# Optimization experiments

Measured on AMD Instinct MI355X. Metric: run time of the kernel, lower is better.

## Reference

```python
import jax, jax.numpy as jnp
import numpy as np

N_PTS = 65536   # input points
M = 4096        # sampled clusters (n_nodes)
K = 16          # knn neighbors
C_IN = 128
C_OUT = 256
BN_EPS = 1e-5


def setup_inputs() -> dict:
    key = jax.random.key(0)
    k1, k2, k3 = jax.random.split(key, 3)
    x = jax.random.normal(k1, (N_PTS, C_IN), jnp.float32)
    pos = jax.random.normal(k2, (N_PTS, 3), jnp.float32)
    batch = jnp.zeros((N_PTS,), jnp.int32)  # single point cloud
    W = jax.random.normal(k3, (C_IN, C_OUT), jnp.float32) / np.sqrt(C_IN)
    b = jnp.zeros((C_OUT,), jnp.float32)
    gamma = jnp.ones((C_OUT,), jnp.float32)
    beta = jnp.zeros((C_OUT,), jnp.float32)
    return {"x": x, "pos": pos, "batch": batch, "W": W, "b": b,
            "gamma": gamma, "beta": beta}


def _fps(pos, m):
    """Farthest point sampling starting from index 0. Returns m indices."""
    n = pos.shape[0]

    def step(carry, _):
        min_d, last = carry
        d = jnp.sum((pos - pos[last]) ** 2, axis=-1)  # [N]
        min_d = jnp.minimum(min_d, d)
        nxt = jnp.argmax(min_d).astype(jnp.int32)
        return (min_d, nxt), nxt

    init = (jnp.full((n,), jnp.inf, pos.dtype), jnp.int32(0))
    _, rest = jax.lax.scan(step, init, None, length=m - 1)
    return jnp.concatenate([jnp.zeros((1,), jnp.int32), rest])


def _knn(pos, sub_pos, k):
    """For each of M query points, indices of k nearest points in pos. [M, k]"""
    # squared euclidean distances, [M, N]
    d2 = (jnp.sum(sub_pos ** 2, -1, keepdims=True)
          - 2.0 * sub_pos @ pos.T
          + jnp.sum(pos ** 2, -1)[None, :])
    _, idx = jax.lax.top_k(-d2, k)
    return idx


def _mlp(x, W, b, gamma, beta):
    # Linear -> BatchNorm1d (training-mode batch stats, biased var) -> ReLU
    h = x @ W + b                      # [N, C_OUT]
    mu = jnp.mean(h, axis=0)
    var = jnp.mean((h - mu) ** 2, axis=0)
    h = gamma * (h - mu) * jax.lax.rsqrt(var + BN_EPS) + beta
    return jax.nn.relu(h)


def reference(x, pos, batch, W, b, gamma, beta):
    id_clusters = _fps(pos, M)                 # [M]
    sub_pos = pos[id_clusters]                 # [M, 3]
    sub_batch = batch[id_clusters]             # [M]
    nbr = _knn(pos, sub_pos, K)                # [M, K]
    h = _mlp(x, W, b, gamma, beta)             # [N, C_OUT]
    # gather + max-pool over each cluster's k neighbors (== scatter_max,
    # since knn emits exactly K neighbors per cluster, grouped by cluster)
    out = jnp.max(h[nbr], axis=1)              # [M, C_OUT]
    return out, sub_pos, sub_batch
```

## Files before the change

kernel.cpp:

```cpp
#include <hip/hip_runtime.h>
#include <hip/hip_bf16.h>

#define N_PTS 65536
#define MCLUS 4096
#define KNN   16
#define C_IN  128
#define C_OUT 256

typedef unsigned long long u64;
typedef unsigned u32;

#define WS_ID     0
#define WS_SLOTS  16384
#define WS_BBOX   49152
#define WS_CNT    49216
#define WS_OFS    180288
#define WS_NBR    49216
#define WS_POS4   311360
#define WS_PSUM   311360
#define WS_PSUMSQ 835648
#define WS_SCALE  1359936
#define WS_SHIFT  1360960

__device__ __forceinline__ u32 fkey(float v) {
    u32 u = __float_as_uint(v);
    return (u >> 31) ? ~u : (u | 0x80000000u);
}
__device__ __forceinline__ float funkey(u32 k) {
    u32 u = (k >> 31) ? (k & 0x7FFFFFFFu) : ~k;
    return __uint_as_float(u);
}

__global__ void init_kernel(int* __restrict__ id, u64* __restrict__ slots,
                            u32* __restrict__ bbox, int* __restrict__ cellcnt) {
    int t = threadIdx.x;
    for (int i = t; i < 4096; i += 1024) slots[i] = 0ull;
    for (int i = t; i < 32768; i += 1024) cellcnt[i] = 0;
    if (t < 3)   bbox[t] = 0xFFFFFFFFu;
    if (t >= 3 && t < 6) bbox[t] = 0u;
    if (t == 0) id[0] = 0;
}

__global__ __launch_bounds__(256) void bbox_kernel(const float* __restrict__ pos,
                                                   u32* __restrict__ bbox) {
    int t = blockIdx.x * 256 + threadIdx.x;
    u32 mn0 = 0xFFFFFFFFu, mn1 = 0xFFFFFFFFu, mn2 = 0xFFFFFFFFu;
    u32 mx0 = 0u, mx1 = 0u, mx2 = 0u;
    for (int i = t; i < N_PTS; i += 16384) {
        u32 k0 = fkey(pos[i*3+0]), k1 = fkey(pos[i*3+1]), k2 = fkey(pos[i*3+2]);
        mn0 = min(mn0, k0); mn1 = min(mn1, k1); mn2 = min(mn2, k2);
        mx0 = max(mx0, k0); mx1 = max(mx1, k1); mx2 = max(mx2, k2);
    }
    #pragma unroll
    for (int off = 32; off > 0; off >>= 1) {
        mn0 = min(mn0, (u32)__shfl_xor(mn0, off)); mx0 = max(mx0, (u32)__shfl_xor(mx0, off));
        mn1 = min(mn1, (u32)__shfl_xor(mn1, off)); mx1 = max(mx1, (u32)__shfl_xor(mx1, off));
        mn2 = min(mn2, (u32)__shfl_xor(mn2, off)); mx2 = max(mx2, (u32)__shfl_xor(mx2, off));
    }
    if ((threadIdx.x & 63) == 0) {
        atomicMin(&bbox[0], mn0); atomicMin(&bbox[1], mn1); atomicMin(&bbox[2], mn2);
        atomicMax(&bbox[3], mx0); atomicMax(&bbox[4], mx1); atomicMax(&bbox[5], mx2);
    }
}

__device__ __forceinline__ int cell_of(float x, float y, float z, const u32* bb) {
    float x0 = funkey(bb[0]), y0 = funkey(bb[1]), z0 = funkey(bb[2]);
    float x1 = funkey(bb[3]), y1 = funkey(bb[4]), z1 = funkey(bb[5]);
    float sx = 32.0f / fmaxf(x1 - x0, 1e-20f);
    float sy = 32.0f / fmaxf(y1 - y0, 1e-20f);
    float sz = 32.0f / fmaxf(z1 - z0, 1e-20f);
    int gx = min(max((int)((x - x0) * sx), 0), 31);
    int gy = min(max((int)((y - y0) * sy), 0), 31);
    int gz = min(max((int)((z - z0) * sz), 0), 31);
    int m = 0;
    #pragma unroll
    for (int k = 0; k < 5; ++k)
        m |= (((gx >> k) & 1) << (3*k + 2)) | (((gy >> k) & 1) << (3*k + 1)) | (((gz >> k) & 1) << (3*k));
    return m;
}

__global__ __launch_bounds__(256) void count_kernel(const float* __restrict__ pos,
                                                    const u32* __restrict__ bbox,
                                                    int* __restrict__ cellcnt) {
    int i = blockIdx.x * 256 + threadIdx.x;
    atomicAdd(&cellcnt[cell_of(pos[i*3+0], pos[i*3+1], pos[i*3+2], bbox)], 1);
}

__global__ __launch_bounds__(1024) void scan_kernel(const int* __restrict__ cellcnt,
                                                    int* __restrict__ cellofs) {
    __shared__ int ts[1024];
    int t = threadIdx.x;
    int v[32]; int s = 0;
    #pragma unroll
    for (int i = 0; i < 32; ++i) { v[i] = cellcnt[t*32 + i]; s += v[i]; }
    ts[t] = s; __syncthreads();
    for (int off = 1; off < 1024; off <<= 1) {
        int u = (t >= off) ? ts[t - off] : 0;
        __syncthreads();
        ts[t] += u;
        __syncthreads();
    }
    int pre = (t == 0) ? 0 : ts[t - 1];
    #pragma unroll
    for (int i = 0; i < 32; ++i) { cellofs[t*32 + i] = pre; pre += v[i]; }
}

__global__ __launch_bounds__(256) void scatter_kernel(const float* __restrict__ pos,
                                                      const u32* __restrict__ bbox,
                                                      int* __restrict__ cellofs,
                                                      float4* __restrict__ pos4) {
    int i = blockIdx.x * 256 + threadIdx.x;
    float x = pos[i*3+0], y = pos[i*3+1], z = pos[i*3+2];
    int o = atomicAdd(&cellofs[cell_of(x, y, z, bbox)], 1);
    pos4[o] = make_float4(x, y, z, __int_as_float(i));
}

__device__ __forceinline__ float dist3(float ax, float ay, float az,
                                       float bx, float by, float bz) {
    float dx = __fsub_rn(ax, bx), dy = __fsub_rn(ay, by), dz = __fsub_rn(az, bz);
    return __fadd_rn(__fadd_rn(__fmul_rn(dx, dx), __fmul_rn(dy, dy)), __fmul_rn(dz, dz));
}

__device__ __forceinline__ u32 wave_max_u32(u32 v) {
    #pragma unroll
    for (int off = 32; off > 0; off >>= 1) {
        u32 o = __shfl_xor(v, off);
        v = o > v ? o : v;
    }
    return v;
}
__device__ __forceinline__ u32 wave_min_u32(u32 v) {
    #pragma unroll
    for (int off = 32; off > 0; off >>= 1) {
        u32 o = __shfl_xor(v, off);
        v = o < v ? o : v;
    }
    return v;
}

__device__ __forceinline__ int wave_argmax48(u64 k48) {
    u32 hi = (u32)(k48 >> 16);
    u32 him = wave_max_u32(hi);
    u64 ball = __ballot(hi == him);
    if (__popcll(ball) > 1) {
        u32 a = (hi == him) ? (u32)(k48 & 0xFFFFull) : 0u;
        u32 am = wave_max_u32(a);
        ball = __ballot((hi == him) && (a == am));
    }
    return __ffsll((long long)ball) - 1;
}

__global__ __launch_bounds__(64) void fps_kernel(const float* __restrict__ pos,
                                                 const float4* __restrict__ pos4,
                                                 int* __restrict__ id,
                                                 u64* __restrict__ slots) {
    const int lane = threadIdx.x;
    const int blk  = blockIdx.x;
    __shared__ float bku[1024];

    float px[16], py[16], pz[16], md[16];
    u32 inv[16];
    const float c0x = pos[0], c0y = pos[1], c0z = pos[2];
    #pragma unroll
    for (int e = 0; e < 16; ++e) {
        int sp = blk * 1024 + (lane >> 3) * 128 + e * 8 + (lane & 7);
        float4 v = pos4[sp];
        px[e] = v.x; py[e] = v.y; pz[e] = v.z;
        inv[e] = 0xFFFFu - (u32)__float_as_int(v.w);
        md[e] = dist3(px[e], py[e], pz[e], c0x, c0y, c0z);
    }

    int r = 0;
    u32 fb_mine = 0xFu;

    auto slow_round = [&](int rr, int s) {
        u64 bk = 0; float bx = 0.f, by = 0.f, bz = 0.f;
        #pragma unroll
        for (int e = 0; e < 16; ++e) {
            u64 k = ((u64)__float_as_uint(md[e]) << 16) | inv[e];
            bool bt = k > bk;
            bk = bt ? k : bk; bx = bt ? px[e] : bx; by = bt ? py[e] : by; bz = bt ? pz[e] : bz;
        }
        int src = wave_argmax48(bk);
        float wx = __shfl(bx, src), wy = __shfl(by, src), wz = __shfl(bz, src);
        u64 kb = __shfl(bk, src);

        const u64 tg = (u64)((rr + 1) & 0xFFFF);
        u64* base = &slots[(u32)(rr & 1) * 2048];
        {
            u64 w0 = (kb << 16) | tg;
            u64 w1 = ((u64)__float_as_uint(wx) << 32) | tg;
            u64 w2 = ((u64)__float_as_uint(wy) << 32) | tg;
            u64 w3 = ((u64)__float_as_uint(wz) << 32) | tg;
            u64 wv = (lane == 0) ? w0 : (lane == 1) ? w1 : (lane == 2) ? w2 : w3;
            if (lane < 4)
                __hip_atomic_store(&base[(u32)blk * 32 + (u32)lane], wv,
                                   __ATOMIC_RELAXED, __HIP_MEMORY_SCOPE_AGENT);
        }
        u64* bp = &base[(u32)lane * 32];
        u64 v0, v1, v2, v3;
        for (;;) {
            v0 = __hip_atomic_load(&bp[0], __ATOMIC_RELAXED, __HIP_MEMORY_SCOPE_AGENT);
            v1 = __hip_atomic_load(&bp[1], __ATOMIC_RELAXED, __HIP_MEMORY_SCOPE_AGENT);
            v2 = __hip_atomic_load(&bp[2], __ATOMIC_RELAXED, __HIP_MEMORY_SCOPE_AGENT);
            v3 = __hip_atomic_load(&bp[3], __ATOMIC_RELAXED, __HIP_MEMORY_SCOPE_AGENT);
            u64 bad = ((v0 ^ tg) | (v1 ^ tg) | (v2 ^ tg) | (v3 ^ tg)) & 0xFFFFull;
            if (bad == 0ull) break;
        }
        u64 k2 = v0 >> 16;
        int s2 = wave_argmax48(k2);
        u64 kw = __shfl(k2, s2);
        float cx = __shfl(__uint_as_float((u32)(v1 >> 32)), s2);
        float cy = __shfl(__uint_as_float((u32)(v2 >> 32)), s2);
        float cz = __shfl(__uint_as_float((u32)(v3 >> 32)), s2);
        if (blk == 0 && lane == 0) id[s] = (int)(0xFFFFu - (u32)(kw & 0xFFFFull));
        #pragma unroll
        for (int e = 0; e < 16; ++e)
            md[e] = fminf(md[e], dist3(px[e], py[e], pz[e], cx, cy, cz));
    };

    u64 wk48[8]; float wxa[8], wya[8], wza[8];

    for (int B = 0; B <= 511; ++B) {
        u64 bk = 0; float bx = 0.f, by = 0.f, bz = 0.f;
        #pragma unroll
        for (int e = 0; e < 16; ++e) {
            u64 k = ((u64)__float_as_uint(md[e]) << 16) | inv[e];
            bool bt = k > bk;
            bk = bt ? k : bk; bx = bt ? px[e] : bx; by = bt ? py[e] : by; bz = bt ? pz[e] : bz;
        }
        u64 ks = bk;
        #pragma unroll
        for (int off = 1; off <= 4; off <<= 1) {
            u64 o = __shfl_xor(ks, off);
            if (o > ks) ks = o;
        }
        {
            u64 ball = __ballot(bk == ks);
            int segbase = (lane >> 3) << 3;
            int ssrc = __ffsll((long long)(ball & (0xFFull << segbase))) - 1;
            bx = __shfl(bx, ssrc); by = __shfl(by, ssrc); bz = __shfl(bz, ssrc);
        }

        const u64 tg = (u64)((r + 1) & 0xFFFF);
        u64* base = &slots[(u32)(r & 1) * 2048];
        {
            int c = lane / 3; if (c > 7) c = 7;
            int p = lane - c * 3;
            int srcl = 8 * c;
            u64 kk  = __shfl(ks, srcl);
            float gx = __shfl(bx, srcl), gy = __shfl(by, srcl), gz = __shfl(bz, srcl);
            u32 hi, mid;
            if (p == 0)      { hi = __float_as_uint(gx); mid = (u32)(kk & 0xFFFFull); }
            else if (p == 1) { hi = __float_as_uint(gy); mid = (u32)(kk >> 32) & 0xFFFFu; }
            else             { hi = __float_as_uint(gz); mid = (u32)(kk >> 16) & 0xFFFFu; }
            u64 wd = ((u64)hi << 32) | ((u64)mid << 16) | tg;
            if (lane == 24) wd = ((u64)(fb_mine & 0xFu) << 16) | tg;
            if (lane < 25)
                __hip_atomic_store(&base[(u32)blk * 32 + (u32)lane], wd,
                                   __ATOMIC_RELAXED, __HIP_MEMORY_SCOPE_AGENT);
        }

        u64 w[25]; u32 valid = 0;
        {
            u64* bp = &base[(u32)lane * 32];
            do {
                #pragma unroll
                for (int i = 0; i < 25; ++i)
                    if (!(valid & (1u << i)))
                        w[i] = __hip_atomic_load(&bp[i], __ATOMIC_RELAXED, __HIP_MEMORY_SCOPE_AGENT);
                #pragma unroll
                for (int i = 0; i < 25; ++i)
                    if ((u32)(w[i] & 0xFFFFull) == (u32)tg) valid |= (1u << i);
            } while (valid != 0x1FFFFFFu);
        }
        ++r;

        u32 jstar = wave_min_u32((u32)(w[24] >> 16) & 0xFu);
        if (jstar < 8u) {
            #pragma unroll
            for (int e = 0; e < 16; ++e) md[e] = bku[e * 64 + lane];
            #pragma unroll
            for (int j = 0; j < 8; ++j) {
                if ((u32)j < jstar) {
                    #pragma unroll
                    for (int e = 0; e < 16; ++e)
                        md[e] = fminf(md[e], dist3(px[e], py[e], pz[e], wxa[j], wya[j], wza[j]));
                }
            }
            int sbase = 8 * (B - 1) + 1;
            for (int sub = (int)jstar; sub < 8; ++sub) { slow_round(r, sbase + sub); ++r; }
            fb_mine = 0xFu;
            --B; continue;
        }
        if (B == 511) break;

        float cpx[8], cpy[8], cpz[8], cmdf[8]; u32 cinv[8];
        #pragma unroll
        for (int c = 0; c < 8; ++c) {
            u64 a = w[3 * c], b = w[3 * c + 1], d = w[3 * c + 2];
            cpx[c] = __uint_as_float((u32)(a >> 32));
            cpy[c] = __uint_as_float((u32)(b >> 32));
            cpz[c] = __uint_as_float((u32)(d >> 32));
            cinv[c] = (u32)(a >> 16) & 0xFFFFu;
            u32 mdb = (((u32)(b >> 16) & 0xFFFFu) << 16) | ((u32)(d >> 16) & 0xFFFFu);
            cmdf[c] = __uint_as_float(mdb);
        }

        float pwx = 0.f, pwy = 0.f, pwz = 0.f;
        #pragma unroll
        for (int j = 0; j < 8; ++j) {
            if (j) {
                #pragma unroll
                for (int c = 0; c < 8; ++c)
                    cmdf[c] = fminf(cmdf[c], dist3(cpx[c], cpy[c], cpz[c], pwx, pwy, pwz));
            }
            u64 bk2 = 0; float b2x = 0.f, b2y = 0.f, b2z = 0.f;
            #pragma unroll
            for (int c = 0; c < 8; ++c) {
                u64 k = ((u64)__float_as_uint(cmdf[c]) << 16) | cinv[c];
                bool bt = k > bk2;
                bk2 = bt ? k : bk2; b2x = bt ? cpx[c] : b2x; b2y = bt ? cpy[c] : b2y; b2z = bt ? cpz[c] : b2z;
            }
            int src = wave_argmax48(bk2);
            u64 kw = __shfl(bk2, src);
            float wx = __shfl(b2x, src), wy = __shfl(b2y, src), wz = __shfl(b2z, src);
            wk48[j] = kw; wxa[j] = wx; wya[j] = wy; wza[j] = wz;
            pwx = wx; pwy = wy; pwz = wz;
            if (blk == 0 && lane == 0) id[8 * B + 1 + j] = (int)(0xFFFFu - (u32)(kw & 0xFFFFull));
        }

        #pragma unroll
        for (int e = 0; e < 16; ++e) bku[e * 64 + lane] = md[e];
        u32 vmask = 0;
        #pragma unroll
        for (int j = 0; j < 8; ++j) {
            #pragma unroll
            for (int e = 0; e < 16; ++e) {
                u64 vk = ((u64)__float_as_uint(md[e]) << 16) | inv[e];
                if (vk > wk48[j]) vmask |= (1u << j);
            }
            #pragma unroll
            for (int e = 0; e < 16; ++e)
                md[e] = fminf(md[e], dist3(px[e], py[e], pz[e], wxa[j], wya[j], wza[j]));
        }
        #pragma unroll
        for (int off = 32; off > 0; off >>= 1) vmask |= (u32)__shfl_xor(vmask, off);
        fb_mine = vmask ? (u32)(__ffs(vmask) - 1) : 0xFu;
    }

    for (int s = 4089; s < 4096; ++s) { slow_round(r, s); ++r; }
}

__global__ void subout_kernel(const float* __restrict__ pos, const int* __restrict__ batch,
                              const int* __restrict__ id, float* __restrict__ sub_pos,
                              int* __restrict__ sub_batch) {
    int m = blockIdx.x * blockDim.x + threadIdx.x;
    if (m >= MCLUS) return;
    int idx = id[m];
    sub_pos[m*3+0] = pos[idx*3+0];
    sub_pos[m*3+1] = pos[idx*3+1];
    sub_pos[m*3+2] = pos[idx*3+2];
    sub_batch[m] = batch[idx];
}

__global__ __launch_bounds__(64) void knn_kernel(const float* __restrict__ pos,
                                                 const int* __restrict__ id,
                                                 int* __restrict__ nbr) {
    const int q = blockIdx.x;
    const int lane = threadIdx.x;
    const int qi = id[q];
    const float qx = pos[qi*3+0], qy = pos[qi*3+1], qz = pos[qi*3+2];
    const float nq = __fadd_rn(__fadd_rn(__fmul_rn(qx,qx), __fmul_rn(qy,qy)), __fmul_rn(qz,qz));

    float dl[KNN]; int il[KNN];
    #pragma unroll
    for (int t = 0; t < KNN; ++t) { dl[t] = __builtin_inff(); il[t] = 0x7FFFFFFF; }

    for (int j = lane; j < N_PTS; j += 64) {
        float px = pos[j*3+0], py = pos[j*3+1], pz = pos[j*3+2];
        float npj = __fadd_rn(__fadd_rn(__fmul_rn(px,px), __fmul_rn(py,py)), __fmul_rn(pz,pz));
        float dot = __fadd_rn(__fadd_rn(__fmul_rn(qx,px), __fmul_rn(qy,py)), __fmul_rn(qz,pz));
        float d2  = __fadd_rn(__fsub_rn(nq, __fmul_rn(2.0f, dot)), npj);
        if (d2 < dl[KNN-1] || (d2 == dl[KNN-1] && j < il[KNN-1])) {
            dl[KNN-1] = d2; il[KNN-1] = j;
            #pragma unroll
            for (int t = KNN-1; t > 0; --t) {
                float a = dl[t-1], bq = dl[t];
                int   ai = il[t-1], bi = il[t];
                bool sw = (bq < a) || (bq == a && bi < ai);
                dl[t-1] = sw ? bq : a;  dl[t] = sw ? a : bq;
                il[t-1] = sw ? bi : ai; il[t] = sw ? ai : bi;
            }
        }
    }

    __shared__ float sd[64][KNN];
    __shared__ int   si[64][KNN];
    #pragma unroll
    for (int t = 0; t < KNN; ++t) { sd[lane][t] = dl[t]; si[lane][t] = il[t]; }
    __syncthreads();

    int ptr = 0;
    for (int rr = 0; rr < KNN; ++rr) {
        unsigned long long key = ~0ull;
        if (ptr < KNN) {
            unsigned u = __float_as_uint(sd[lane][ptr]);
            unsigned mu = (u >> 31) ? ~u : (u | 0x80000000u);
            key = ((unsigned long long)mu << 32) | (unsigned)si[lane][ptr];
        }
        unsigned long long m = key;
        #pragma unroll
        for (int off = 32; off > 0; off >>= 1) {
            unsigned long long o = __shfl_xor(m, off);
            if (o < m) m = o;
        }
        if (key == m) ptr++;
        if (lane == 0) nbr[q*KNN + rr] = (int)(m & 0xFFFFFFFFull);
    }
}

__global__ __launch_bounds__(256) void stats_kernel(const float* __restrict__ x,
                                                    const float* __restrict__ W,
                                                    const float* __restrict__ b,
                                                    float* __restrict__ psum,
                                                    float* __restrict__ psumsq) {
    __shared__ float xl[64*128];
    const int tid = threadIdx.x;
    const int cg = (tid & 63) * 4;
    const int rq = tid >> 6;
    float s0=0,s1=0,s2v=0,s3=0, q0=0,q1=0,q2=0,q3=0;
    const float4 bv = *(const float4*)&b[cg];

    for (int t = 0; t < 2; ++t) {
        const size_t row0 = (size_t)blockIdx.x*128 + (size_t)t*64;
        __syncthreads();
        for (int i = tid*4; i < 64*128; i += 1024)
            *(float4*)&xl[i] = *(const float4*)&x[row0*128 + i];
        __syncthreads();

        float acc[16][4];
        #pragma unroll
        for (int rr = 0; rr < 16; ++rr) { acc[rr][0]=bv.x; acc[rr][1]=bv.y; acc[rr][2]=bv.z; acc[rr][3]=bv.w; }

        for (int k4 = 0; k4 < 32; ++k4) {
            float4 w0 = *(const float4*)&W[(k4*4+0)*256 + cg];
            float4 w1 = *(const float4*)&W[(k4*4+1)*256 + cg];
            float4 w2 = *(const float4*)&W[(k4*4+2)*256 + cg];
            float4 w3 = *(const float4*)&W[(k4*4+3)*256 + cg];
            #pragma unroll
            for (int rr = 0; rr < 16; ++rr) {
                float4 xv = *(float4*)&xl[(rq*16+rr)*128 + k4*4];
                acc[rr][0] = fmaf(xv.w,w3.x, fmaf(xv.z,w2.x, fmaf(xv.y,w1.x, fmaf(xv.x,w0.x, acc[rr][0]))));
                acc[rr][1] = fmaf(xv.w,w3.y, fmaf(xv.z,w2.y, fmaf(xv.y,w1.y, fmaf(xv.x,w0.y, acc[rr][1]))));
                acc[rr][2] = fmaf(xv.w,w3.z, fmaf(xv.z,w2.z, fmaf(xv.y,w1.z, fmaf(xv.x,w0.z, acc[rr][2]))));
                acc[rr][3] = fmaf(xv.w,w3.w, fmaf(xv.z,w2.w, fmaf(xv.y,w1.w, fmaf(xv.x,w0.w, acc[rr][3]))));
            }
        }
        #pragma unroll
        for (int rr = 0; rr < 16; ++rr) {
            s0 += acc[rr][0]; q0 = fmaf(acc[rr][0],acc[rr][0],q0);
            s1 += acc[rr][1]; q1 = fmaf(acc[rr][1],acc[rr][1],q1);
            s2v+= acc[rr][2]; q2 = fmaf(acc[rr][2],acc[rr][2],q2);
            s3 += acc[rr][3]; q3 = fmaf(acc[rr][3],acc[rr][3],q3);
        }
    }
    __syncthreads();
    float* red = xl;
    red[rq*256 + cg+0] = s0; red[rq*256 + cg+1] = s1; red[rq*256 + cg+2] = s2v; red[rq*256 + cg+3] = s3;
    red[1024 + rq*256 + cg+0] = q0; red[1024 + rq*256 + cg+1] = q1;
    red[1024 + rq*256 + cg+2] = q2; red[1024 + rq*256 + cg+3] = q3;
    __syncthreads();
    if (rq == 0) {
        #pragma unroll
        for (int c = 0; c < 4; ++c) {
            int ch = cg + c;
            float ss = red[ch] + red[256+ch] + red[512+ch] + red[768+ch];
            float qq = red[1024+ch] + red[1280+ch] + red[1536+ch] + red[1792+ch];
            psum  [blockIdx.x*256 + ch] = ss;
            psumsq[blockIdx.x*256 + ch] = qq;
        }
    }
}

__global__ void finalize_kernel(const float* __restrict__ psum, const float* __restrict__ psumsq,
                                const float* __restrict__ gamma, const float* __restrict__ beta,
                                float* __restrict__ scale, float* __restrict__ shift) {
    int c = threadIdx.x;
    float s = 0.f, s2 = 0.f;
    for (int bl = 0; bl < 512; ++bl) { s += psum[bl*256+c]; s2 += psumsq[bl*256+c]; }
    float mu  = s  / 65536.0f;
    float var = s2 / 65536.0f - mu*mu;
    float inv = rsqrtf(var + 1e-5f);
    float sc = gamma[c] * inv;
    scale[c] = sc;
    shift[c] = beta[c] - mu * sc;
}

__global__ __launch_bounds__(256) void out_kernel(const float* __restrict__ x,
                                                  const float* __restrict__ W,
                                                  const float* __restrict__ b,
                                                  const int* __restrict__ nbr,
                                                  const float* __restrict__ scale,
                                                  const float* __restrict__ shift,
                                                  float* __restrict__ out) {
    __shared__ float xl[16*128];
    __shared__ int nb[16];
    const int tid = threadIdx.x;
    const int m = blockIdx.x;
    if (tid < 16) nb[tid] = nbr[m*16 + tid];
    __syncthreads();
    for (int i = tid; i < 16*128; i += 256) {
        int rr = i >> 7, k = i & 127;
        xl[i] = x[(size_t)nb[rr]*128 + k];
    }
    __syncthreads();

    float acc[16];
    const float bias = b[tid];
    #pragma unroll
    for (int rr = 0; rr < 16; ++rr) acc[rr] = bias;

    for (int k4 = 0; k4 < 32; ++k4) {
        float w0 = W[(k4*4+0)*256 + tid];
        float w1 = W[(k4*4+1)*256 + tid];
        float w2 = W[(k4*4+2)*256 + tid];
        float w3 = W[(k4*4+3)*256 + tid];
        #pragma unroll
        for (int rr = 0; rr < 16; ++rr) {
            float4 xv = *(float4*)&xl[rr*128 + k4*4];
            acc[rr] = fmaf(xv.w,w3, fmaf(xv.z,w2, fmaf(xv.y,w1, fmaf(xv.x,w0, acc[rr]))));
        }
    }
    const float sc = scale[tid], sh = shift[tid];
    float v = acc[0];
    #pragma unroll
    for (int rr = 1; rr < 16; ++rr) v = (sc >= 0.f) ? fmaxf(v, acc[rr]) : fminf(v, acc[rr]);
    out[(size_t)m*256 + tid] = fmaxf(fmaf(sc, v, sh), 0.f);
}

extern "C" void kernel_launch(void* const* d_in, const int* in_sizes, int n_in,
                              void* d_out, int out_size, void* d_ws, size_t ws_size,
                              hipStream_t stream) {
    const float* x     = (const float*)d_in[0];
    const float* pos   = (const float*)d_in[1];
    const int*   batch = (const int*)  d_in[2];
    const float* W     = (const float*)d_in[3];
    const float* b     = (const float*)d_in[4];
    const float* gamma = (const float*)d_in[5];
    const float* beta  = (const float*)d_in[6];

    float* out      = (float*)d_out;
    float* sub_pos  = out + (size_t)MCLUS*C_OUT;
    int*   sub_batch= (int*)(out + (size_t)MCLUS*C_OUT + (size_t)MCLUS*3);

    char* ws = (char*)d_ws;
    int*    id      = (int*)   (ws + WS_ID);
    u64*    slots   = (u64*)   (ws + WS_SLOTS);
    u32*    bbox    = (u32*)   (ws + WS_BBOX);
    int*    cellcnt = (int*)   (ws + WS_CNT);
    int*    cellofs = (int*)   (ws + WS_OFS);
    int*    nbr     = (int*)   (ws + WS_NBR);
    float4* pos4    = (float4*)(ws + WS_POS4);
    float*  psum    = (float*) (ws + WS_PSUM);
    float*  psumsq  = (float*) (ws + WS_PSUMSQ);
    float*  scalep  = (float*) (ws + WS_SCALE);
    float*  shiftp  = (float*) (ws + WS_SHIFT);

    init_kernel<<<1, 1024, 0, stream>>>(id, slots, bbox, cellcnt);
    bbox_kernel<<<64, 256, 0, stream>>>(pos, bbox);
    count_kernel<<<256, 256, 0, stream>>>(pos, bbox, cellcnt);
    scan_kernel<<<1, 1024, 0, stream>>>(cellcnt, cellofs);
    scatter_kernel<<<256, 256, 0, stream>>>(pos, bbox, cellofs, pos4);
    fps_kernel<<<64, 64, 0, stream>>>(pos, pos4, id, slots);
    subout_kernel<<<16, 256, 0, stream>>>(pos, batch, id, sub_pos, sub_batch);
    knn_kernel<<<MCLUS, 64, 0, stream>>>(pos, id, nbr);
    stats_kernel<<<512, 256, 0, stream>>>(x, W, b, psum, psumsq);
    finalize_kernel<<<1, 256, 0, stream>>>(psum, psumsq, gamma, beta, scalep, shiftp);
    out_kernel<<<MCLUS, 256, 0, stream>>>(x, W, b, nbr, scalep, shiftp, out);
}
```

Before: 7.829 ms.

## Rewrite FPS as single-block bounding-box-pruned segment update

Replaces the 64-block FPS, which used cross-block atomic slot exchange and speculative 8-step batching, with a single 1024-thread block. Points are split into 512 spatially sorted segments, each with a bounding box and a cached champion. Each step only updates segments whose bounding box lies closer to the new centre than their current max distance. This removes grid-wide spin synchronisation and skips distance updates for unaffected segments. In exchange, all work runs on one CU, min-distances move to global memory, and there are two block barriers per step.

```diff
diff --git a/kernel.cpp b/kernel.cpp
--- a/kernel.cpp
+++ b/kernel.cpp
@@ -9,12 +9,13 @@
 
 typedef unsigned long long u64;
 typedef unsigned u32;
+typedef unsigned short u16;
 
 #define WS_ID     0
-#define WS_SLOTS  16384
-#define WS_BBOX   49152
+#define WS_BBOX   16384
 #define WS_CNT    49216
 #define WS_OFS    180288
+#define WS_MDG    49216
 #define WS_NBR    49216
 #define WS_POS4   311360
 #define WS_PSUM   311360
@@ -31,10 +32,9 @@
     return __uint_as_float(u);
 }
 
-__global__ void init_kernel(int* __restrict__ id, u64* __restrict__ slots,
-                            u32* __restrict__ bbox, int* __restrict__ cellcnt) {
+__global__ void init_kernel(int* __restrict__ id, u32* __restrict__ bbox,
+                            int* __restrict__ cellcnt) {
     int t = threadIdx.x;
-    for (int i = t; i < 4096; i += 1024) slots[i] = 0ull;
     for (int i = t; i < 32768; i += 1024) cellcnt[i] = 0;
     if (t < 3)   bbox[t] = 0xFFFFFFFFu;
     if (t >= 3 && t < 6) bbox[t] = 0u;
@@ -121,235 +121,115 @@
     return __fadd_rn(__fadd_rn(__fmul_rn(dx, dx), __fmul_rn(dy, dy)), __fmul_rn(dz, dz));
 }
 
-__device__ __forceinline__ u32 wave_max_u32(u32 v) {
-    #pragma unroll
-    for (int off = 32; off > 0; off >>= 1) {
-        u32 o = __shfl_xor(v, off);
-        v = o > v ? o : v;
-    }
-    return v;
-}
-__device__ __forceinline__ u32 wave_min_u32(u32 v) {
-    #pragma unroll
-    for (int off = 32; off > 0; off >>= 1) {
-        u32 o = __shfl_xor(v, off);
-        v = o < v ? o : v;
-    }
-    return v;
-}
-
-__device__ __forceinline__ int wave_argmax48(u64 k48) {
-    u32 hi = (u32)(k48 >> 16);
-    u32 him = wave_max_u32(hi);
-    u64 ball = __ballot(hi == him);
-    if (__popcll(ball) > 1) {
-        u32 a = (hi == him) ? (u32)(k48 & 0xFFFFull) : 0u;
-        u32 am = wave_max_u32(a);
-        ball = __ballot((hi == him) && (a == am));
-    }
-    return __ffsll((long long)ball) - 1;
-}
-
-__global__ __launch_bounds__(64) void fps_kernel(const float* __restrict__ pos,
-                                                 const float4* __restrict__ pos4,
-                                                 int* __restrict__ id,
-                                                 u64* __restrict__ slots) {
-    const int lane = threadIdx.x;
-    const int blk  = blockIdx.x;
-    __shared__ float bku[1024];
-
-    float px[16], py[16], pz[16], md[16];
-    u32 inv[16];
+__global__ __launch_bounds__(1024) void fps_kernel(const float* __restrict__ pos,
+                                                   const float4* __restrict__ pos4,
+                                                   float* __restrict__ mdg,
+                                                   int* __restrict__ id) {
+    const int tid = threadIdx.x;
+    const int wave = tid >> 6, lane = tid & 63;
+    __shared__ float bax[512], bay[512], baz[512], bbx[512], bby[512], bbz[512];
+    __shared__ u64 champ[512];
+    __shared__ float chx[512], chy[512], chz[512];
+    __shared__ u16 wl[2][512];
+    __shared__ int wlc[2];
+
     const float c0x = pos[0], c0y = pos[1], c0z = pos[2];
-    #pragma unroll
-    for (int e = 0; e < 16; ++e) {
-        int sp = blk * 1024 + (lane >> 3) * 128 + e * 8 + (lane & 7);
-        float4 v = pos4[sp];
-        px[e] = v.x; py[e] = v.y; pz[e] = v.z;
-        inv[e] = 0xFFFFu - (u32)__float_as_int(v.w);
-        md[e] = dist3(px[e], py[e], pz[e], c0x, c0y, c0z);
-    }
-
-    int r = 0;
-    u32 fb_mine = 0xFu;
-
-    auto slow_round = [&](int rr, int s) {
-        u64 bk = 0; float bx = 0.f, by = 0.f, bz = 0.f;
-        #pragma unroll
-        for (int e = 0; e < 16; ++e) {
-            u64 k = ((u64)__float_as_uint(md[e]) << 16) | inv[e];
-            bool bt = k > bk;
-            bk = bt ? k : bk; bx = bt ? px[e] : bx; by = bt ? py[e] : by; bz = bt ? pz[e] : bz;
-        }
-        int src = wave_argmax48(bk);
-        float wx = __shfl(bx, src), wy = __shfl(by, src), wz = __shfl(bz, src);
-        u64 kb = __shfl(bk, src);
-
-        const u64 tg = (u64)((rr + 1) & 0xFFFF);
-        u64* base = &slots[(u32)(rr & 1) * 2048];
-        {
-            u64 w0 = (kb << 16) | tg;
-            u64 w1 = ((u64)__float_as_uint(wx) << 32) | tg;
-            u64 w2 = ((u64)__float_as_uint(wy) << 32) | tg;
-            u64 w3 = ((u64)__float_as_uint(wz) << 32) | tg;
-            u64 wv = (lane == 0) ? w0 : (lane == 1) ? w1 : (lane == 2) ? w2 : w3;
-            if (lane < 4)
-                __hip_atomic_store(&base[(u32)blk * 32 + (u32)lane], wv,
-                                   __ATOMIC_RELAXED, __HIP_MEMORY_SCOPE_AGENT);
-        }
-        u64* bp = &base[(u32)lane * 32];
-        u64 v0, v1, v2, v3;
-        for (;;) {
-            v0 = __hip_atomic_load(&bp[0], __ATOMIC_RELAXED, __HIP_MEMORY_SCOPE_AGENT);
-            v1 = __hip_atomic_load(&bp[1], __ATOMIC_RELAXED, __HIP_MEMORY_SCOPE_AGENT);
-            v2 = __hip_atomic_load(&bp[2], __ATOMIC_RELAXED, __HIP_MEMORY_SCOPE_AGENT);
-            v3 = __hip_atomic_load(&bp[3], __ATOMIC_RELAXED, __HIP_MEMORY_SCOPE_AGENT);
-            u64 bad = ((v0 ^ tg) | (v1 ^ tg) | (v2 ^ tg) | (v3 ^ tg)) & 0xFFFFull;
-            if (bad == 0ull) break;
-        }
-        u64 k2 = v0 >> 16;
-        int s2 = wave_argmax48(k2);
-        u64 kw = __shfl(k2, s2);
-        float cx = __shfl(__uint_as_float((u32)(v1 >> 32)), s2);
-        float cy = __shfl(__uint_as_float((u32)(v2 >> 32)), s2);
-        float cz = __shfl(__uint_as_float((u32)(v3 >> 32)), s2);
-        if (blk == 0 && lane == 0) id[s] = (int)(0xFFFFu - (u32)(kw & 0xFFFFull));
-        #pragma unroll
-        for (int e = 0; e < 16; ++e)
-            md[e] = fminf(md[e], dist3(px[e], py[e], pz[e], cx, cy, cz));
-    };
-
-    u64 wk48[8]; float wxa[8], wya[8], wza[8];
-
-    for (int B = 0; B <= 511; ++B) {
-        u64 bk = 0; float bx = 0.f, by = 0.f, bz = 0.f;
-        #pragma unroll
-        for (int e = 0; e < 16; ++e) {
-            u64 k = ((u64)__float_as_uint(md[e]) << 16) | inv[e];
-            bool bt = k > bk;
-            bk = bt ? k : bk; bx = bt ? px[e] : bx; by = bt ? py[e] : by; bz = bt ? pz[e] : bz;
-        }
-        u64 ks = bk;
-        #pragma unroll
-        for (int off = 1; off <= 4; off <<= 1) {
-            u64 o = __shfl_xor(ks, off);
-            if (o > ks) ks = o;
-        }
-        {
-            u64 ball = __ballot(bk == ks);
-            int segbase = (lane >> 3) << 3;
-            int ssrc = __ffsll((long long)(ball & (0xFFull << segbase))) - 1;
-            bx = __shfl(bx, ssrc); by = __shfl(by, ssrc); bz = __shfl(bz, ssrc);
-        }
-
-        const u64 tg = (u64)((r + 1) & 0xFFFF);
-        u64* base = &slots[(u32)(r & 1) * 2048];
-        {
-            int c = lane / 3; if (c > 7) c = 7;
-            int p = lane - c * 3;
-            int srcl = 8 * c;
-            u64 kk  = __shfl(ks, srcl);
-            float gx = __shfl(bx, srcl), gy = __shfl(by, srcl), gz = __shfl(bz, srcl);
-            u32 hi, mid;
-            if (p == 0)      { hi = __float_as_uint(gx); mid = (u32)(kk & 0xFFFFull); }
-            else if (p == 1) { hi = __float_as_uint(gy); mid = (u32)(kk >> 32) & 0xFFFFu; }
-            else             { hi = __float_as_uint(gz); mid = (u32)(kk >> 16) & 0xFFFFu; }
-            u64 wd = ((u64)hi << 32) | ((u64)mid << 16) | tg;
-            if (lane == 24) wd = ((u64)(fb_mine & 0xFu) << 16) | tg;
-            if (lane < 25)
-                __hip_atomic_store(&base[(u32)blk * 32 + (u32)lane], wd,
-                                   __ATOMIC_RELAXED, __HIP_MEMORY_SCOPE_AGENT);
-        }
-
-        u64 w[25]; u32 valid = 0;
-        {
-            u64* bp = &base[(u32)lane * 32];
-            do {
-                #pragma unroll
-                for (int i = 0; i < 25; ++i)
-                    if (!(valid & (1u << i)))
-                        w[i] = __hip_atomic_load(&bp[i], __ATOMIC_RELAXED, __HIP_MEMORY_SCOPE_AGENT);
-                #pragma unroll
-                for (int i = 0; i < 25; ++i)
-                    if ((u32)(w[i] & 0xFFFFull) == (u32)tg) valid |= (1u << i);
-            } while (valid != 0x1FFFFFFu);
-        }
-        ++r;
-
-        u32 jstar = wave_min_u32((u32)(w[24] >> 16) & 0xFu);
-        if (jstar < 8u) {
+
+    for (int seg = wave; seg < 512; seg += 16) {
+        int p0 = seg*128 + lane, p1 = p0 + 64;
+        float4 a = pos4[p0], b = pos4[p1];
+        float m0 = dist3(a.x, a.y, a.z, c0x, c0y, c0z);
+        float m1 = dist3(b.x, b.y, b.z, c0x, c0y, c0z);
+        mdg[p0] = m0; mdg[p1] = m1;
+        float xn = fminf(a.x,b.x), xM = fmaxf(a.x,b.x);
+        float yn = fminf(a.y,b.y), yM = fmaxf(a.y,b.y);
+        float zn = fminf(a.z,b.z), zM = fmaxf(a.z,b.z);
+        u64 k0 = ((u64)__float_as_uint(m0) << 16) | (0xFFFFu - (u32)__float_as_int(a.w));
+        u64 k1 = ((u64)__float_as_uint(m1) << 16) | (0xFFFFu - (u32)__float_as_int(b.w));
+        bool t = k1 > k0;
+        u64 kk = t ? k1 : k0;
+        float qx = t ? b.x : a.x, qy = t ? b.y : a.y, qz = t ? b.z : a.z;
+        #pragma unroll
+        for (int off = 32; off > 0; off >>= 1) {
+            xn = fminf(xn, (float)__shfl_xor(xn, off)); xM = fmaxf(xM, (float)__shfl_xor(xM, off));
+            yn = fminf(yn, (float)__shfl_xor(yn, off)); yM = fmaxf(yM, (float)__shfl_xor(yM, off));
+            zn = fminf(zn, (float)__shfl_xor(zn, off)); zM = fmaxf(zM, (float)__shfl_xor(zM, off));
+            u64 ok = __shfl_xor(kk, off);
+            float ox = __shfl_xor(qx, off), oy = __shfl_xor(qy, off), oz = __shfl_xor(qz, off);
+            if (ok > kk) { kk = ok; qx = ox; qy = oy; qz = oz; }
+        }
+        if (lane == 0) {
+            bax[seg] = xn; bbx[seg] = xM;
+            bay[seg] = yn; bby[seg] = yM;
+            baz[seg] = zn; bbz[seg] = zM;
+            champ[seg] = kk; chx[seg] = qx; chy[seg] = qy; chz[seg] = qz;
+        }
+    }
+    if (tid == 0) { id[0] = 0; wlc[0] = 0; wlc[1] = 0; }
+    __syncthreads();
+
+    for (int s = 1; s < 4096; ++s) {
+        const int buf = s & 1;
+        u64 kmax = 0; int kseg = 0;
+        #pragma unroll
+        for (int i = 0; i < 8; ++i) {
+            u64 k = champ[lane + 64*i];
+            if (k > kmax) { kmax = k; kseg = lane + 64*i; }
+        }
+        #pragma unroll
+        for (int off = 32; off > 0; off >>= 1) {
+            u64 ok = __shfl_xor(kmax, off);
+            int os = __shfl_xor(kseg, off);
+            if (ok > kmax) { kmax = ok; kseg = os; }
+        }
+        const float cx = chx[kseg], cy = chy[kseg], cz = chz[kseg];
+        if (tid == 0) id[s] = (int)(0xFFFFu - (u32)(kmax & 0xFFFFull));
+        if (s == 4095) break;
+
+        if (tid < 512) {
+            float ddx = fmaxf(fmaxf(bax[tid] - cx, cx - bbx[tid]), 0.f);
+            float ddy = fmaxf(fmaxf(bay[tid] - cy, cy - bby[tid]), 0.f);
+            float ddz = fmaxf(fmaxf(baz[tid] - cz, cz - bbz[tid]), 0.f);
+            float dbb = ddx*ddx + ddy*ddy + ddz*ddz;
+            float cm  = __uint_as_float((u32)(champ[tid] >> 16));
+            bool aff = dbb < cm * 1.00002f;
+            u64 ball = __ballot(aff);
+            int nb = __popcll(ball);
+            int pre = __popcll(ball & ((1ull << lane) - 1ull));
+            int base = 0;
+            if (lane == 0 && nb) base = atomicAdd(&wlc[buf], nb);
+            base = __shfl(base, 0);
+            if (aff) wl[buf][base + pre] = (u16)tid;
+        }
+        if (tid == 0) wlc[buf ^ 1] = 0;
+        __syncthreads();
+
+        const int n = wlc[buf];
+        for (int i = wave; i < n; i += 16) {
+            int seg = wl[buf][i];
+            int p0 = seg*128 + lane, p1 = p0 + 64;
+            float4 a = pos4[p0]; float m0 = mdg[p0];
+            float4 b = pos4[p1]; float m1 = mdg[p1];
+            m0 = fminf(m0, dist3(a.x, a.y, a.z, cx, cy, cz));
+            m1 = fminf(m1, dist3(b.x, b.y, b.z, cx, cy, cz));
+            mdg[p0] = m0; mdg[p1] = m1;
+            u64 k0 = ((u64)__float_as_uint(m0) << 16) | (0xFFFFu - (u32)__float_as_int(a.w));
+            u64 k1 = ((u64)__float_as_uint(m1) << 16) | (0xFFFFu - (u32)__float_as_int(b.w));
+            bool t = k1 > k0;
+            u64 kk = t ? k1 : k0;
+            float qx = t ? b.x : a.x, qy = t ? b.y : a.y, qz = t ? b.z : a.z;
             #pragma unroll
-            for (int e = 0; e < 16; ++e) md[e] = bku[e * 64 + lane];
-            #pragma unroll
-            for (int j = 0; j < 8; ++j) {
-                if ((u32)j < jstar) {
-                    #pragma unroll
-                    for (int e = 0; e < 16; ++e)
-                        md[e] = fminf(md[e], dist3(px[e], py[e], pz[e], wxa[j], wya[j], wza[j]));
-                }
+            for (int off = 32; off > 0; off >>= 1) {
+                u64 ok = __shfl_xor(kk, off);
+                float ox = __shfl_xor(qx, off), oy = __shfl_xor(qy, off), oz = __shfl_xor(qz, off);
+                if (ok > kk) { kk = ok; qx = ox; qy = oy; qz = oz; }
             }
-            int sbase = 8 * (B - 1) + 1;
-            for (int sub = (int)jstar; sub < 8; ++sub) { slow_round(r, sbase + sub); ++r; }
-            fb_mine = 0xFu;
-            --B; continue;
-        }
-        if (B == 511) break;
-
-        float cpx[8], cpy[8], cpz[8], cmdf[8]; u32 cinv[8];
-        #pragma unroll
-        for (int c = 0; c < 8; ++c) {
-            u64 a = w[3 * c], b = w[3 * c + 1], d = w[3 * c + 2];
-            cpx[c] = __uint_as_float((u32)(a >> 32));
-            cpy[c] = __uint_as_float((u32)(b >> 32));
-            cpz[c] = __uint_as_float((u32)(d >> 32));
-            cinv[c] = (u32)(a >> 16) & 0xFFFFu;
-            u32 mdb = (((u32)(b >> 16) & 0xFFFFu) << 16) | ((u32)(d >> 16) & 0xFFFFu);
-            cmdf[c] = __uint_as_float(mdb);
-        }
-
-        float pwx = 0.f, pwy = 0.f, pwz = 0.f;
-        #pragma unroll
-        for (int j = 0; j < 8; ++j) {
-            if (j) {
-                #pragma unroll
-                for (int c = 0; c < 8; ++c)
-                    cmdf[c] = fminf(cmdf[c], dist3(cpx[c], cpy[c], cpz[c], pwx, pwy, pwz));
+            if (lane == 0) {
+                champ[seg] = kk; chx[seg] = qx; chy[seg] = qy; chz[seg] = qz;
             }
-            u64 bk2 = 0; float b2x = 0.f, b2y = 0.f, b2z = 0.f;
-            #pragma unroll
-            for (int c = 0; c < 8; ++c) {
-                u64 k = ((u64)__float_as_uint(cmdf[c]) << 16) | cinv[c];
-                bool bt = k > bk2;
-                bk2 = bt ? k : bk2; b2x = bt ? cpx[c] : b2x; b2y = bt ? cpy[c] : b2y; b2z = bt ? cpz[c] : b2z;
-            }
-            int src = wave_argmax48(bk2);
-            u64 kw = __shfl(bk2, src);
-            float wx = __shfl(b2x, src), wy = __shfl(b2y, src), wz = __shfl(b2z, src);
-            wk48[j] = kw; wxa[j] = wx; wya[j] = wy; wza[j] = wz;
-            pwx = wx; pwy = wy; pwz = wz;
-            if (blk == 0 && lane == 0) id[8 * B + 1 + j] = (int)(0xFFFFu - (u32)(kw & 0xFFFFull));
-        }
-
-        #pragma unroll
-        for (int e = 0; e < 16; ++e) bku[e * 64 + lane] = md[e];
-        u32 vmask = 0;
-        #pragma unroll
-        for (int j = 0; j < 8; ++j) {
-            #pragma unroll
-            for (int e = 0; e < 16; ++e) {
-                u64 vk = ((u64)__float_as_uint(md[e]) << 16) | inv[e];
-                if (vk > wk48[j]) vmask |= (1u << j);
-            }
-            #pragma unroll
-            for (int e = 0; e < 16; ++e)
-                md[e] = fminf(md[e], dist3(px[e], py[e], pz[e], wxa[j], wya[j], wza[j]));
-        }
-        #pragma unroll
-        for (int off = 32; off > 0; off >>= 1) vmask |= (u32)__shfl_xor(vmask, off);
-        fb_mine = vmask ? (u32)(__ffs(vmask) - 1) : 0xFu;
-    }
-
-    for (int s = 4089; s < 4096; ++s) { slow_round(r, s); ++r; }
+        }
+        __syncthreads();
+    }
 }
 
 __global__ void subout_kernel(const float* __restrict__ pos, const int* __restrict__ batch,
@@ -556,10 +436,10 @@
 
     char* ws = (char*)d_ws;
     int*    id      = (int*)   (ws + WS_ID);
-    u64*    slots   = (u64*)   (ws + WS_SLOTS);
     u32*    bbox    = (u32*)   (ws + WS_BBOX);
     int*    cellcnt = (int*)   (ws + WS_CNT);
     int*    cellofs = (int*)   (ws + WS_OFS);
+    float*  mdg     = (float*) (ws + WS_MDG);
     int*    nbr     = (int*)   (ws + WS_NBR);
     float4* pos4    = (float4*)(ws + WS_POS4);
     float*  psum    = (float*) (ws + WS_PSUM);
@@ -567,12 +447,12 @@
     float*  scalep  = (float*) (ws + WS_SCALE);
     float*  shiftp  = (float*) (ws + WS_SHIFT);
 
-    init_kernel<<<1, 1024, 0, stream>>>(id, slots, bbox, cellcnt);
+    init_kernel<<<1, 1024, 0, stream>>>(id, bbox, cellcnt);
     bbox_kernel<<<64, 256, 0, stream>>>(pos, bbox);
     count_kernel<<<256, 256, 0, stream>>>(pos, bbox, cellcnt);
     scan_kernel<<<1, 1024, 0, stream>>>(cellcnt, cellofs);
     scatter_kernel<<<256, 256, 0, stream>>>(pos, bbox, cellofs, pos4);
-    fps_kernel<<<64, 64, 0, stream>>>(pos, pos4, id, slots);
+    fps_kernel<<<1, 1024, 0, stream>>>(pos, pos4, mdg, id);
     subout_kernel<<<16, 256, 0, stream>>>(pos, batch, id, sub_pos, sub_batch);
     knn_kernel<<<MCLUS, 64, 0, stream>>>(pos, id, nbr);
     stats_kernel<<<512, 256, 0, stream>>>(x, W, b, psum, psumsq);
```

Result: slower. 16.71 ms (+113.4%).

## Replace slow-round fallback with variable-length speculative batches in FPS

Applied to the files above, without the earlier changes.

The persistent FPS kernel now commits only the verified prefix of each speculative batch of 8 picks. It then restarts speculation from that point, instead of falling back to single-pick rounds that each need a full cross-block exchange. The fixed-length block loop and the tail of slow rounds are replaced by a running count of confirmed samples and a variable batch size. This is meant to cut the number of global synchronization rounds after mis-speculation and at the tail. In exchange the control flow is more complex, and a conflict now always costs an extra exchange round before progress resumes.

```diff
diff --git a/kernel.cpp b/kernel.cpp
--- a/kernel.cpp
+++ b/kernel.cpp
@@ -172,56 +172,11 @@
 
     int r = 0;
     u32 fb_mine = 0xFu;
-
-    auto slow_round = [&](int rr, int s) {
-        u64 bk = 0; float bx = 0.f, by = 0.f, bz = 0.f;
-        #pragma unroll
-        for (int e = 0; e < 16; ++e) {
-            u64 k = ((u64)__float_as_uint(md[e]) << 16) | inv[e];
-            bool bt = k > bk;
-            bk = bt ? k : bk; bx = bt ? px[e] : bx; by = bt ? py[e] : by; bz = bt ? pz[e] : bz;
-        }
-        int src = wave_argmax48(bk);
-        float wx = __shfl(bx, src), wy = __shfl(by, src), wz = __shfl(bz, src);
-        u64 kb = __shfl(bk, src);
-
-        const u64 tg = (u64)((rr + 1) & 0xFFFF);
-        u64* base = &slots[(u32)(rr & 1) * 2048];
-        {
-            u64 w0 = (kb << 16) | tg;
-            u64 w1 = ((u64)__float_as_uint(wx) << 32) | tg;
-            u64 w2 = ((u64)__float_as_uint(wy) << 32) | tg;
-            u64 w3 = ((u64)__float_as_uint(wz) << 32) | tg;
-            u64 wv = (lane == 0) ? w0 : (lane == 1) ? w1 : (lane == 2) ? w2 : w3;
-            if (lane < 4)
-                __hip_atomic_store(&base[(u32)blk * 32 + (u32)lane], wv,
-                                   __ATOMIC_RELAXED, __HIP_MEMORY_SCOPE_AGENT);
-        }
-        u64* bp = &base[(u32)lane * 32];
-        u64 v0, v1, v2, v3;
-        for (;;) {
-            v0 = __hip_atomic_load(&bp[0], __ATOMIC_RELAXED, __HIP_MEMORY_SCOPE_AGENT);
-            v1 = __hip_atomic_load(&bp[1], __ATOMIC_RELAXED, __HIP_MEMORY_SCOPE_AGENT);
-            v2 = __hip_atomic_load(&bp[2], __ATOMIC_RELAXED, __HIP_MEMORY_SCOPE_AGENT);
-            v3 = __hip_atomic_load(&bp[3], __ATOMIC_RELAXED, __HIP_MEMORY_SCOPE_AGENT);
-            u64 bad = ((v0 ^ tg) | (v1 ^ tg) | (v2 ^ tg) | (v3 ^ tg)) & 0xFFFFull;
-            if (bad == 0ull) break;
-        }
-        u64 k2 = v0 >> 16;
-        int s2 = wave_argmax48(k2);
-        u64 kw = __shfl(k2, s2);
-        float cx = __shfl(__uint_as_float((u32)(v1 >> 32)), s2);
-        float cy = __shfl(__uint_as_float((u32)(v2 >> 32)), s2);
-        float cz = __shfl(__uint_as_float((u32)(v3 >> 32)), s2);
-        if (blk == 0 && lane == 0) id[s] = (int)(0xFFFFu - (u32)(kw & 0xFFFFull));
-        #pragma unroll
-        for (int e = 0; e < 16; ++e)
-            md[e] = fminf(md[e], dist3(px[e], py[e], pz[e], cx, cy, cz));
-    };
-
+    int s_conf = 0;
+    int nsub = 0;
     u64 wk48[8]; float wxa[8], wya[8], wza[8];
 
-    for (int B = 0; B <= 511; ++B) {
+    for (;;) {
         u64 bk = 0; float bx = 0.f, by = 0.f, bz = 0.f;
         #pragma unroll
         for (int e = 0; e < 16; ++e) {
@@ -277,23 +232,24 @@
         ++r;
 
         u32 jstar = wave_min_u32((u32)(w[24] >> 16) & 0xFu);
-        if (jstar < 8u) {
+        int adv = (jstar < (u32)nsub) ? (int)jstar : nsub;
+        if (adv < nsub) {
             #pragma unroll
             for (int e = 0; e < 16; ++e) md[e] = bku[e * 64 + lane];
             #pragma unroll
             for (int j = 0; j < 8; ++j) {
-                if ((u32)j < jstar) {
+                if (j < adv) {
                     #pragma unroll
                     for (int e = 0; e < 16; ++e)
                         md[e] = fminf(md[e], dist3(px[e], py[e], pz[e], wxa[j], wya[j], wza[j]));
                 }
             }
-            int sbase = 8 * (B - 1) + 1;
-            for (int sub = (int)jstar; sub < 8; ++sub) { slow_round(r, sbase + sub); ++r; }
-            fb_mine = 0xFu;
-            --B; continue;
-        }
-        if (B == 511) break;
+            s_conf += adv; nsub = 0; fb_mine = 0xFu;
+            continue;
+        }
+        s_conf += nsub; nsub = 0; fb_mine = 0xFu;
+        if (s_conf >= 4095) break;
+        nsub = (4095 - s_conf) < 8 ? (4095 - s_conf) : 8;
 
         float cpx[8], cpy[8], cpz[8], cmdf[8]; u32 cinv[8];
         #pragma unroll
@@ -307,49 +263,52 @@
             cmdf[c] = __uint_as_float(mdb);
         }
 
+        #pragma unroll
+        for (int e = 0; e < 16; ++e) bku[e * 64 + lane] = md[e];
+
         float pwx = 0.f, pwy = 0.f, pwz = 0.f;
         #pragma unroll
         for (int j = 0; j < 8; ++j) {
-            if (j) {
+            if (j < nsub) {
+                if (j) {
+                    #pragma unroll
+                    for (int c = 0; c < 8; ++c)
+                        cmdf[c] = fminf(cmdf[c], dist3(cpx[c], cpy[c], cpz[c], pwx, pwy, pwz));
+                }
+                u64 bk2 = 0; float b2x = 0.f, b2y = 0.f, b2z = 0.f;
                 #pragma unroll
-                for (int c = 0; c < 8; ++c)
-                    cmdf[c] = fminf(cmdf[c], dist3(cpx[c], cpy[c], cpz[c], pwx, pwy, pwz));
+                for (int c = 0; c < 8; ++c) {
+                    u64 k = ((u64)__float_as_uint(cmdf[c]) << 16) | cinv[c];
+                    bool bt = k > bk2;
+                    bk2 = bt ? k : bk2; b2x = bt ? cpx[c] : b2x; b2y = bt ? cpy[c] : b2y; b2z = bt ? cpz[c] : b2z;
+                }
+                int src = wave_argmax48(bk2);
+                u64 kw = __shfl(bk2, src);
+                float wx = __shfl(b2x, src), wy = __shfl(b2y, src), wz = __shfl(b2z, src);
+                wk48[j] = kw; wxa[j] = wx; wya[j] = wy; wza[j] = wz;
+                pwx = wx; pwy = wy; pwz = wz;
+                if (blk == 0 && lane == 0) id[s_conf + 1 + j] = (int)(0xFFFFu - (u32)(kw & 0xFFFFull));
             }
-            u64 bk2 = 0; float b2x = 0.f, b2y = 0.f, b2z = 0.f;
-            #pragma unroll
-            for (int c = 0; c < 8; ++c) {
-                u64 k = ((u64)__float_as_uint(cmdf[c]) << 16) | cinv[c];
-                bool bt = k > bk2;
-                bk2 = bt ? k : bk2; b2x = bt ? cpx[c] : b2x; b2y = bt ? cpy[c] : b2y; b2z = bt ? cpz[c] : b2z;
+        }
+
+        u32 vmask = 0;
+        #pragma unroll
+        for (int j = 0; j < 8; ++j) {
+            if (j < nsub) {
+                #pragma unroll
+                for (int e = 0; e < 16; ++e) {
+                    u64 vk = ((u64)__float_as_uint(md[e]) << 16) | inv[e];
+                    if (vk > wk48[j]) vmask |= (1u << j);
+                }
+                #pragma unroll
+                for (int e = 0; e < 16; ++e)
+                    md[e] = fminf(md[e], dist3(px[e], py[e], pz[e], wxa[j], wya[j], wza[j]));
             }
-            int src = wave_argmax48(bk2);
-            u64 kw = __shfl(bk2, src);
-            float wx = __shfl(b2x, src), wy = __shfl(b2y, src), wz = __shfl(b2z, src);
-            wk48[j] = kw; wxa[j] = wx; wya[j] = wy; wza[j] = wz;
-            pwx = wx; pwy = wy; pwz = wz;
-            if (blk == 0 && lane == 0) id[8 * B + 1 + j] = (int)(0xFFFFu - (u32)(kw & 0xFFFFull));
-        }
-
-        #pragma unroll
-        for (int e = 0; e < 16; ++e) bku[e * 64 + lane] = md[e];
-        u32 vmask = 0;
-        #pragma unroll
-        for (int j = 0; j < 8; ++j) {
-            #pragma unroll
-            for (int e = 0; e < 16; ++e) {
-                u64 vk = ((u64)__float_as_uint(md[e]) << 16) | inv[e];
-                if (vk > wk48[j]) vmask |= (1u << j);
-            }
-            #pragma unroll
-            for (int e = 0; e < 16; ++e)
-                md[e] = fminf(md[e], dist3(px[e], py[e], pz[e], wxa[j], wya[j], wza[j]));
         }
         #pragma unroll
         for (int off = 32; off > 0; off >>= 1) vmask |= (u32)__shfl_xor(vmask, off);
         fb_mine = vmask ? (u32)(__ffs(vmask) - 1) : 0xFu;
     }
-
-    for (int s = 4089; s < 4096; ++s) { slow_round(r, s); ++r; }
 }
 
 __global__ void subout_kernel(const float* __restrict__ pos, const int* __restrict__ batch,
```

New measurement: 8.062 ms. +3.0%, slower.

## Resume speculative FPS batches after one slow round instead of finishing the batch serially

Applied to the files above, without the earlier changes.

The speculative 8-wide farthest-point-sampling loop now tracks a confirmed-sample counter instead of a fixed batch index. On a mis-speculation it accepts the verified prefix, runs a single exact slow round, and then returns to speculative batching rather than running slow rounds for the rest of the batch. The final partial batch is handled by shrinking the batch size, so the trailing serial slow rounds go away. This is meant to cut the number of slow grid-synchronised rounds, at the cost of more complex control flow and per-j predication.

```diff
diff --git a/kernel.cpp b/kernel.cpp
--- a/kernel.cpp
+++ b/kernel.cpp
@@ -172,6 +172,9 @@
 
     int r = 0;
     u32 fb_mine = 0xFu;
+    int s_conf = 0;
+    int nsub = 0;
+    u64 wk48[8]; float wxa[8], wya[8], wza[8];
 
     auto slow_round = [&](int rr, int s) {
         u64 bk = 0; float bx = 0.f, by = 0.f, bz = 0.f;
@@ -219,9 +222,7 @@
             md[e] = fminf(md[e], dist3(px[e], py[e], pz[e], cx, cy, cz));
     };
 
-    u64 wk48[8]; float wxa[8], wya[8], wza[8];
-
-    for (int B = 0; B <= 511; ++B) {
+    for (;;) {
         u64 bk = 0; float bx = 0.f, by = 0.f, bz = 0.f;
         #pragma unroll
         for (int e = 0; e < 16; ++e) {
@@ -277,23 +278,30 @@
         ++r;
 
         u32 jstar = wave_min_u32((u32)(w[24] >> 16) & 0xFu);
-        if (jstar < 8u) {
+        int adv = (jstar < (u32)nsub) ? (int)jstar : nsub;
+        if (adv < nsub) {
             #pragma unroll
             for (int e = 0; e < 16; ++e) md[e] = bku[e * 64 + lane];
             #pragma unroll
             for (int j = 0; j < 8; ++j) {
-                if ((u32)j < jstar) {
+                if (j < adv) {
                     #pragma unroll
                     for (int e = 0; e < 16; ++e)
                         md[e] = fminf(md[e], dist3(px[e], py[e], pz[e], wxa[j], wya[j], wza[j]));
                 }
             }
-            int sbase = 8 * (B - 1) + 1;
-            for (int sub = (int)jstar; sub < 8; ++sub) { slow_round(r, sbase + sub); ++r; }
-            fb_mine = 0xFu;
-            --B; continue;
-        }
-        if (B == 511) break;
+            s_conf += adv; nsub = 0; fb_mine = 0xFu;
+            if (s_conf < 4095) {
+                slow_round(r, s_conf + 1);
+                ++r;
+                s_conf += 1;
+            }
+            if (s_conf >= 4095) break;
+            continue;
+        }
+        s_conf += nsub; nsub = 0; fb_mine = 0xFu;
+        if (s_conf >= 4095) break;
+        nsub = (4095 - s_conf) < 8 ? (4095 - s_conf) : 8;
 
         float cpx[8], cpy[8], cpz[8], cmdf[8]; u32 cinv[8];
         #pragma unroll
@@ -307,49 +315,52 @@
             cmdf[c] = __uint_as_float(mdb);
         }
 
+        #pragma unroll
+        for (int e = 0; e < 16; ++e) bku[e * 64 + lane] = md[e];
+
         float pwx = 0.f, pwy = 0.f, pwz = 0.f;
         #pragma unroll
         for (int j = 0; j < 8; ++j) {
-            if (j) {
+            if (j < nsub) {
+                if (j) {
+                    #pragma unroll
+                    for (int c = 0; c < 8; ++c)
+                        cmdf[c] = fminf(cmdf[c], dist3(cpx[c], cpy[c], cpz[c], pwx, pwy, pwz));
+                }
+                u64 bk2 = 0; float b2x = 0.f, b2y = 0.f, b2z = 0.f;
                 #pragma unroll
-                for (int c = 0; c < 8; ++c)
-                    cmdf[c] = fminf(cmdf[c], dist3(cpx[c], cpy[c], cpz[c], pwx, pwy, pwz));
+                for (int c = 0; c < 8; ++c) {
+                    u64 k = ((u64)__float_as_uint(cmdf[c]) << 16) | cinv[c];
+                    bool bt = k > bk2;
+                    bk2 = bt ? k : bk2; b2x = bt ? cpx[c] : b2x; b2y = bt ? cpy[c] : b2y; b2z = bt ? cpz[c] : b2z;
+                }
+                int src = wave_argmax48(bk2);
+                u64 kw = __shfl(bk2, src);
+                float wx = __shfl(b2x, src), wy = __shfl(b2y, src), wz = __shfl(b2z, src);
+                wk48[j] = kw; wxa[j] = wx; wya[j] = wy; wza[j] = wz;
+                pwx = wx; pwy = wy; pwz = wz;
+                if (blk == 0 && lane == 0) id[s_conf + 1 + j] = (int)(0xFFFFu - (u32)(kw & 0xFFFFull));
             }
-            u64 bk2 = 0; float b2x = 0.f, b2y = 0.f, b2z = 0.f;
-            #pragma unroll
-            for (int c = 0; c < 8; ++c) {
-                u64 k = ((u64)__float_as_uint(cmdf[c]) << 16) | cinv[c];
-                bool bt = k > bk2;
-                bk2 = bt ? k : bk2; b2x = bt ? cpx[c] : b2x; b2y = bt ? cpy[c] : b2y; b2z = bt ? cpz[c] : b2z;
+        }
+
+        u32 vmask = 0;
+        #pragma unroll
+        for (int j = 0; j < 8; ++j) {
+            if (j < nsub) {
+                #pragma unroll
+                for (int e = 0; e < 16; ++e) {
+                    u64 vk = ((u64)__float_as_uint(md[e]) << 16) | inv[e];
+                    if (vk > wk48[j]) vmask |= (1u << j);
+                }
+                #pragma unroll
+                for (int e = 0; e < 16; ++e)
+                    md[e] = fminf(md[e], dist3(px[e], py[e], pz[e], wxa[j], wya[j], wza[j]));
             }
-            int src = wave_argmax48(bk2);
-            u64 kw = __shfl(bk2, src);
-            float wx = __shfl(b2x, src), wy = __shfl(b2y, src), wz = __shfl(b2z, src);
-            wk48[j] = kw; wxa[j] = wx; wya[j] = wy; wza[j] = wz;
-            pwx = wx; pwy = wy; pwz = wz;
-            if (blk == 0 && lane == 0) id[8 * B + 1 + j] = (int)(0xFFFFu - (u32)(kw & 0xFFFFull));
-        }
-
-        #pragma unroll
-        for (int e = 0; e < 16; ++e) bku[e * 64 + lane] = md[e];
-        u32 vmask = 0;
-        #pragma unroll
-        for (int j = 0; j < 8; ++j) {
-            #pragma unroll
-            for (int e = 0; e < 16; ++e) {
-                u64 vk = ((u64)__float_as_uint(md[e]) << 16) | inv[e];
-                if (vk > wk48[j]) vmask |= (1u << j);
-            }
-            #pragma unroll
-            for (int e = 0; e < 16; ++e)
-                md[e] = fminf(md[e], dist3(px[e], py[e], pz[e], wxa[j], wya[j], wza[j]));
         }
         #pragma unroll
         for (int off = 32; off > 0; off >>= 1) vmask |= (u32)__shfl_xor(vmask, off);
         fb_mine = vmask ? (u32)(__ffs(vmask) - 1) : 0xFu;
     }
-
-    for (int s = 4089; s < 4096; ++s) { slow_round(r, s); ++r; }
 }
 
 __global__ void subout_kernel(const float* __restrict__ pos, const int* __restrict__ batch,
```

Result: slower. 8.263 ms (+5.5%).
